# Kernel optimization log

Hardware: AMD Instinct MI355X
Metric: run time of the kernel (lower is better)

## Reference

```python
import jax, jax.numpy as jnp
import numpy as np

IN_CH, OUT_CH = 32, 32
MODES1, MODES2 = 16, 16
B, L, H, W = 8, 16, 64, 33


def setup_inputs() -> dict:
    key = jax.random.key(0)
    k = jax.random.split(key, 6)
    scale = 1.0 / (IN_CH * OUT_CH)
    wshape = (IN_CH, OUT_CH, MODES1, MODES2)
    return {
        "x_re": jax.random.normal(k[0], (B, L, IN_CH, H, W), dtype=jnp.float32),
        "x_im": jax.random.normal(k[1], (B, L, IN_CH, H, W), dtype=jnp.float32),
        "w1_re": scale * jax.random.normal(k[2], wshape, dtype=jnp.float32),
        "w1_im": scale * jax.random.normal(k[3], wshape, dtype=jnp.float32),
        "w2_re": scale * jax.random.normal(k[4], wshape, dtype=jnp.float32),
        "w2_im": scale * jax.random.normal(k[5], wshape, dtype=jnp.float32),
    }


def _mul2d(x, w):
    # x: [B, L, C_in, m1, m2] complex; w: [C_in, C_out, m1, m2] complex
    return jnp.einsum("blcij,coij->bloij", x, w)


def reference(x_re, x_im, w1_re, w1_im, w2_re, w2_im):
    x = jax.lax.complex(x_re, x_im)          # [B, L, C, H, W] complex64
    w1 = jax.lax.complex(w1_re, w1_im)       # [C_in, C_out, m1, m2]
    w2 = jax.lax.complex(w2_re, w2_im)
    Bx, Lx, Cx, Hx, Wx = x.shape
    m1 = min(Hx, MODES1)
    m2 = min(Wx, MODES2)

    out = jnp.zeros((Bx, Lx, OUT_CH, Hx, Wx), dtype=x.dtype)
    # low positive frequencies (top-left corner)
    out = out.at[:, :, :, :m1, :m2].set(
        _mul2d(x[:, :, :, :m1, :m2], w1[:, :, :m1, :m2]))
    # low negative frequencies along H (bottom-left corner)
    if Hx > 1 and (Hx > MODES1 or Wx > MODES2):
        out = out.at[:, :, :, -m1:, :m2].set(
            _mul2d(x[:, :, :, -m1:, :m2], w2[:, :, :m1, :m2]))
    # return complex result as trailing real/imag dim (float32)
    return jnp.stack([out.real, out.imag], axis=-1)
```

## Files before the change

kernel.cpp:

```cpp
#include <hip/hip_runtime.h>

#define IN_CH 32
#define OUT_CH 32
#define M1 16
#define M2 16
#define H_ 64
#define W_ 33
#define HW (H_*W_)
#define BLPB 4
#define WSTRIDE (OUT_CH*M1*M2)

__global__ __launch_bounds__(256) void spectral_fused(
    const float* __restrict__ x_re, const float* __restrict__ x_im,
    const float* __restrict__ w1_re, const float* __restrict__ w1_im,
    const float* __restrict__ w2_re, const float* __restrict__ w2_im,
    float* __restrict__ out)
{
    const int tid = threadIdx.x;

    if (blockIdx.x & 1) {
        const int fid = blockIdx.x >> 1;
        const int gtid = fid * 256 + tid;
        const int nthreads = 1024 * 256;

        float4* out4 = (float4*)out;
        const float4 z4 = make_float4(0.f, 0.f, 0.f, 0.f);
        const int totalA = 4096 * 528;
        for (int idx = gtid; idx < totalA; idx += nthreads) {
            int plane = idx / 528;
            int k = idx - plane * 528;
            out4[(long)plane * 1056 + 264 + k] = z4;
        }
        float2* out2 = (float2*)out;
        const float2 z2 = make_float2(0.f, 0.f);
        const int totalB = 4096 * 544;
        for (int idx = gtid; idx < totalB; idx += nthreads) {
            int plane = idx / 544;
            int r = idx - plane * 544;
            int hh = r / 17;
            int t = r - hh * 17;
            int h = hh < 16 ? hh : hh + 32;
            out2[(long)plane * 2112 + h * 33 + 16 + t] = z2;
        }
        return;
    }

    const int cid = blockIdx.x >> 1;
    const int ri = cid >> 5;
    const int chunk = cid & 31;
    const int region = ri >> 4;
    const int i = ri & 15;
    const int h = region ? (48 + i) : i;
    const int bl0 = chunk * BLPB;

    __shared__ float2 xs[BLPB][IN_CH][M2];

    for (int item = tid; item < BLPB * IN_CH * M2; item += 256) {
        int j = item & 15;
        int c = (item >> 4) & 31;
        int b = item >> 9;
        long src = (long)((bl0 + b) * IN_CH + c) * HW + (long)h * W_ + j;
        xs[b][c][j] = make_float2(x_re[src], x_im[src]);
    }
    __syncthreads();

    const int j  = tid & 15;
    const int o0 = tid >> 4;
    const float* __restrict__ wre = (region ? w2_re : w1_re) + (o0 * M1 + i) * M2 + j;
    const float* __restrict__ wim = (region ? w2_im : w1_im) + (o0 * M1 + i) * M2 + j;

    float2 acc0[BLPB], acc1[BLPB];
    #pragma unroll
    for (int b = 0; b < BLPB; ++b) {
        acc0[b] = make_float2(0.f, 0.f);
        acc1[b] = make_float2(0.f, 0.f);
    }

    #pragma unroll 8
    for (int c = 0; c < IN_CH; ++c) {
        int idx = c * WSTRIDE;
        float wr0 = wre[idx],        wi0 = wim[idx];
        float wr1 = wre[idx + 4096], wi1 = wim[idx + 4096];
        #pragma unroll
        for (int b = 0; b < BLPB; ++b) {
            float2 xc = xs[b][c][j];
            acc0[b].x = fmaf(xc.x, wr0, acc0[b].x); acc0[b].x = fmaf(-xc.y, wi0, acc0[b].x);
            acc0[b].y = fmaf(xc.x, wi0, acc0[b].y); acc0[b].y = fmaf( xc.y, wr0, acc0[b].y);
            acc1[b].x = fmaf(xc.x, wr1, acc1[b].x); acc1[b].x = fmaf(-xc.y, wi1, acc1[b].x);
            acc1[b].y = fmaf(xc.x, wi1, acc1[b].y); acc1[b].y = fmaf( xc.y, wr1, acc1[b].y);
        }
    }

    float2* out2 = (float2*)out;
    #pragma unroll
    for (int b = 0; b < BLPB; ++b) {
        long plane = (long)(bl0 + b) * OUT_CH;
        long d0 = (plane + o0)      * HW + (long)h * W_ + j;
        long d1 = (plane + o0 + 16) * HW + (long)h * W_ + j;
        out2[d0] = acc0[b];
        out2[d1] = acc1[b];
    }
}

extern "C" void kernel_launch(void* const* d_in, const int* in_sizes, int n_in,
                              void* d_out, int out_size, void* d_ws, size_t ws_size,
                              hipStream_t stream) {
    const float* x_re  = (const float*)d_in[0];
    const float* x_im  = (const float*)d_in[1];
    const float* w1_re = (const float*)d_in[2];
    const float* w1_im = (const float*)d_in[3];
    const float* w2_re = (const float*)d_in[4];
    const float* w2_im = (const float*)d_in[5];
    float* out = (float*)d_out;

    spectral_fused<<<dim3(2048), dim3(256), 0, stream>>>(
        x_re, x_im, w1_re, w1_im, w2_re, w2_im, out);
}
```

Before: 37.83 us.

## Retile spectral multiply with 8 BL per block, float4 weight loads and packed FMA

Each compute block now covers 8 batch-time slices instead of 4, and each thread owns one output channel, four modes and four slices. Weights are read as float4 vectors and prefetched one input channel ahead, and shared-memory x is read as float4. The complex multiply-add uses two-wide vector FMAs that can map to packed instructions. The grid changes to a 1:2 ratio of compute to zero-fill blocks, so there are half as many compute blocks, each with more work, and the zero-fill work is spread over the same number of blocks as before.

```diff
diff --git a/kernel.cpp b/kernel.cpp
--- a/kernel.cpp
+++ b/kernel.cpp
@@ -7,8 +7,14 @@
 #define H_ 64
 #define W_ 33
 #define HW (H_*W_)
-#define BLPB 4
-#define WSTRIDE (OUT_CH*M1*M2)
+#define BLPB 8
+
+typedef float f2 __attribute__((ext_vector_type(2)));
+
+__device__ __forceinline__ void cmac(f2& acc, float xr, float xi, float wr, float wi) {
+    acc = __builtin_elementwise_fma((f2){xr, xr}, (f2){wr, wi}, acc);
+    acc = __builtin_elementwise_fma((f2){-xi, xi}, (f2){wi, wr}, acc);
+}
 
 __global__ __launch_bounds__(256) void spectral_fused(
     const float* __restrict__ x_re, const float* __restrict__ x_im,
@@ -17,9 +23,11 @@
     float* __restrict__ out)
 {
     const int tid = threadIdx.x;
+    const int bid = blockIdx.x;
+    const int role = bid % 3;
 
-    if (blockIdx.x & 1) {
-        const int fid = blockIdx.x >> 1;
+    if (role) {
+        const int fid = (bid / 3) * 2 + (role - 1);
         const int gtid = fid * 256 + tid;
         const int nthreads = 1024 * 256;
 
@@ -45,15 +53,15 @@
         return;
     }
 
-    const int cid = blockIdx.x >> 1;
-    const int ri = cid >> 5;
-    const int chunk = cid & 31;
+    const int cid = bid / 3;
+    const int ri = cid >> 4;
+    const int chunk = cid & 15;
     const int region = ri >> 4;
     const int i = ri & 15;
     const int h = region ? (48 + i) : i;
     const int bl0 = chunk * BLPB;
 
-    __shared__ float2 xs[BLPB][IN_CH][M2];
+    __shared__ __align__(16) float2 xs[BLPB][IN_CH][M2];
 
     for (int item = tid; item < BLPB * IN_CH * M2; item += 256) {
         int j = item & 15;
@@ -64,41 +72,51 @@
     }
     __syncthreads();
 
-    const int j  = tid & 15;
-    const int o0 = tid >> 4;
-    const float* __restrict__ wre = (region ? w2_re : w1_re) + (o0 * M1 + i) * M2 + j;
-    const float* __restrict__ wim = (region ? w2_im : w1_im) + (o0 * M1 + i) * M2 + j;
+    const int bh = tid >> 7;
+    const int o  = (tid >> 2) & 31;
+    const int jq = tid & 3;
 
-    float2 acc0[BLPB], acc1[BLPB];
+    const float* wreb = region ? w2_re : w1_re;
+    const float* wimb = region ? w2_im : w1_im;
+    const float4* __restrict__ wre4 = (const float4*)wreb + (o * 64 + i * 4 + jq);
+    const float4* __restrict__ wim4 = (const float4*)wimb + (o * 64 + i * 4 + jq);
+
+    f2 acc[4][4];
     #pragma unroll
-    for (int b = 0; b < BLPB; ++b) {
-        acc0[b] = make_float2(0.f, 0.f);
-        acc1[b] = make_float2(0.f, 0.f);
-    }
+    for (int bb = 0; bb < 4; ++bb)
+        #pragma unroll
+        for (int jj = 0; jj < 4; ++jj)
+            acc[bb][jj] = (f2){0.f, 0.f};
 
-    #pragma unroll 8
+    float4 wr = wre4[0], wi = wim4[0];
+    #pragma unroll 4
     for (int c = 0; c < IN_CH; ++c) {
-        int idx = c * WSTRIDE;
-        float wr0 = wre[idx],        wi0 = wim[idx];
-        float wr1 = wre[idx + 4096], wi1 = wim[idx + 4096];
+        float4 wrn, win;
+        if (c < IN_CH - 1) {
+            wrn = wre4[(c + 1) * 2048];
+            win = wim4[(c + 1) * 2048];
+        }
         #pragma unroll
-        for (int b = 0; b < BLPB; ++b) {
-            float2 xc = xs[b][c][j];
-            acc0[b].x = fmaf(xc.x, wr0, acc0[b].x); acc0[b].x = fmaf(-xc.y, wi0, acc0[b].x);
-            acc0[b].y = fmaf(xc.x, wi0, acc0[b].y); acc0[b].y = fmaf( xc.y, wr0, acc0[b].y);
-            acc1[b].x = fmaf(xc.x, wr1, acc1[b].x); acc1[b].x = fmaf(-xc.y, wi1, acc1[b].x);
-            acc1[b].y = fmaf(xc.x, wi1, acc1[b].y); acc1[b].y = fmaf( xc.y, wr1, acc1[b].y);
+        for (int bb = 0; bb < 4; ++bb) {
+            const float4* xp = (const float4*)&xs[bh * 4 + bb][c][jq * 4];
+            float4 x01 = xp[0];
+            float4 x23 = xp[1];
+            cmac(acc[bb][0], x01.x, x01.y, wr.x, wi.x);
+            cmac(acc[bb][1], x01.z, x01.w, wr.y, wi.y);
+            cmac(acc[bb][2], x23.x, x23.y, wr.z, wi.z);
+            cmac(acc[bb][3], x23.z, x23.w, wr.w, wi.w);
         }
+        wr = wrn; wi = win;
     }
 
     float2* out2 = (float2*)out;
     #pragma unroll
-    for (int b = 0; b < BLPB; ++b) {
-        long plane = (long)(bl0 + b) * OUT_CH;
-        long d0 = (plane + o0)      * HW + (long)h * W_ + j;
-        long d1 = (plane + o0 + 16) * HW + (long)h * W_ + j;
-        out2[d0] = acc0[b];
-        out2[d1] = acc1[b];
+    for (int bb = 0; bb < 4; ++bb) {
+        int bl = bl0 + bh * 4 + bb;
+        long rowbase = ((long)(bl * OUT_CH + o) * H_ + h) * W_ + jq * 4;
+        #pragma unroll
+        for (int jj = 0; jj < 4; ++jj)
+            out2[rowbase + jj] = make_float2(acc[bb][jj].x, acc[bb][jj].y);
     }
 }
 
@@ -113,6 +131,6 @@
     const float* w2_im = (const float*)d_in[5];
     float* out = (float*)d_out;
 
-    spectral_fused<<<dim3(2048), dim3(256), 0, stream>>>(
+    spectral_fused<<<dim3(1536), dim3(256), 0, stream>>>(
         x_re, x_im, w1_re, w1_im, w2_re, w2_im, out);
 }
```

Measured after the change: 38.84 us. +2.7%, slower.
